# Kernel tuning notes

Hardware: AMD Instinct MI355X
Metric: run time of the kernel (lower is better)

Reference implementation:

```python
import jax, jax.numpy as jnp
import numpy as np

# Layer node counts: [n0, n1, n2, n3] for a 3-hop sampled subgraph
N_NODES = [524288, 65536, 8192, 1024]
DIMS = [100, 256, 256, 47]


def sage_conv(x_src, x_dst, src, dst, Wl, bl, Wr, n_dst):
    # PyG SAGEConv: lin_l(mean_agg(neighbors)) + lin_r(root)
    msg = x_src[src]                                        # [E, in]
    agg = jax.ops.segment_sum(msg, dst, num_segments=n_dst)  # [n_dst, in]
    cnt = jax.ops.segment_sum(jnp.ones((src.shape[0],), dtype=x_src.dtype), dst,
                              num_segments=n_dst)
    agg = agg / jnp.maximum(cnt, 1.0)[:, None]               # mean, 0-deg -> 0
    return agg @ Wl + bl + x_dst @ Wr


def setup_inputs() -> dict:
    key = jax.random.key(0)
    ks = jax.random.split(key, 20)
    inp = {"x": jax.random.normal(ks[0], (N_NODES[0], DIMS[0]), dtype=jnp.float32)}
    E = [655360, 81920, 10240]
    for i in range(3):
        inp[f"src{i}"] = jax.random.randint(ks[1 + 2 * i], (E[i],), 0, N_NODES[i])
        inp[f"dst{i}"] = jax.random.randint(ks[2 + 2 * i], (E[i],), 0, N_NODES[i + 1])
    for i in range(3):
        fin, fout = DIMS[i], DIMS[i + 1]
        inp[f"Wl{i}"] = jax.random.normal(ks[7 + 3 * i], (fin, fout), jnp.float32) * (1.0 / np.sqrt(fin))
        inp[f"bl{i}"] = jnp.zeros((fout,), jnp.float32)
        inp[f"Wr{i}"] = jax.random.normal(ks[8 + 3 * i], (fin, fout), jnp.float32) * (1.0 / np.sqrt(fin))
    return inp


def reference(x, src0, dst0, src1, dst1, src2, dst2,
              Wl0, bl0, Wr0, Wl1, bl1, Wr1, Wl2, bl2, Wr2):
    srcs = [src0, src1, src2]
    dsts = [dst0, dst1, dst2]
    Wls = [Wl0, Wl1, Wl2]
    bls = [bl0, bl1, bl2]
    Wrs = [Wr0, Wr1, Wr2]
    h = x
    for i in range(3):
        n_dst = N_NODES[i + 1]
        h_dst = h[:n_dst]
        h = sage_conv(h, h_dst, srcs[i], dsts[i], Wls[i], bls[i], Wrs[i], n_dst)
        if i != 2:
            h = jax.nn.relu(h)  # dropout is identity in eval mode
    return jax.nn.log_softmax(h, axis=-1)
```

## Files before the change

kernel.cpp:

```cpp
#include <hip/hip_runtime.h>
#include <math.h>

constexpr int NN1 = 65536, NN2 = 8192, NN3 = 1024;
constexpr int E0 = 655360, E1 = 81920, E2 = 10240;
constexpr int ETOT = E0 + E1 + E2;
constexpr int NTOT = NN1 + NN2 + NN3;

static inline int cdiv(int a, int b) { return (a + b - 1) / b; }

typedef __bf16 bf16x8_t __attribute__((ext_vector_type(8)));
typedef float f32x4_t __attribute__((ext_vector_type(4)));

__device__ __forceinline__ unsigned short f2bf(float f) {
    union { float f; unsigned int u; } v; v.f = f;
    unsigned int r = v.u + 0x7fffu + ((v.u >> 16) & 1u);
    return (unsigned short)(r >> 16);
}
__device__ __forceinline__ float bf2f(unsigned short h) {
    union { unsigned int u; float f; } v; v.u = ((unsigned int)h) << 16;
    return v.f;
}

constexpr int CB = (ETOT + 255) / 256;
__global__ void count_prep(const int* __restrict__ dst0, const int* __restrict__ dst1,
                           const int* __restrict__ dst2, int* __restrict__ cnt,
                           const float* __restrict__ Wl0, const float* __restrict__ Wr0,
                           unsigned short* __restrict__ Wt0a, unsigned short* __restrict__ Wt0b,
                           const float* __restrict__ Wl1, const float* __restrict__ Wr1,
                           unsigned short* __restrict__ Wt1a, unsigned short* __restrict__ Wt1b) {
    int b = blockIdx.x, t = threadIdx.x;
    if (b < CB) {
        int i = b * 256 + t;
        if (i < E0) atomicAdd(&cnt[dst0[i]], 1);
        else if (i < E0 + E1) atomicAdd(&cnt[NN1 + dst1[i - E0]], 1);
        else if (i < ETOT) atomicAdd(&cnt[NN1 + NN2 + dst2[i - E0 - E1]], 1);
        return;
    }
    b -= CB;
    if (b < 128) {
        int idx = b * 256 + t; int n = idx >> 7, k = idx & 127;
        Wt0a[idx] = f2bf(k < 100 ? Wl0[k * 256 + n] : 0.f);
    } else if (b < 256) {
        int idx = (b - 128) * 256 + t; int n = idx >> 7, k = idx & 127;
        Wt0b[idx] = f2bf(k < 100 ? Wr0[k * 256 + n] : 0.f);
    } else if (b < 512) {
        int idx = (b - 256) * 256 + t; int n = idx >> 8, k = idx & 255;
        Wt1a[idx] = f2bf(Wl1[k * 256 + n]);
    } else {
        int idx = (b - 512) * 256 + t; int n = idx >> 8, k = idx & 255;
        Wt1b[idx] = f2bf(Wr1[k * 256 + n]);
    }
}

__global__ __launch_bounds__(1024) void scan1(const int* __restrict__ cnt, int n,
                                              int* __restrict__ ofs, int* __restrict__ sums) {
    __shared__ int s[1024];
    int i = blockIdx.x * 1024 + threadIdx.x;
    int v = (i < n) ? cnt[i] : 0;
    s[threadIdx.x] = v;
    __syncthreads();
    for (int off = 1; off < 1024; off <<= 1) {
        int t = (threadIdx.x >= off) ? s[threadIdx.x - off] : 0;
        __syncthreads();
        s[threadIdx.x] += t;
        __syncthreads();
    }
    if (i < n) ofs[i] = s[threadIdx.x] - v;
    if (threadIdx.x == 1023) sums[blockIdx.x] = s[1023];
}

__global__ void scan3(const int* __restrict__ sums, int n,
                      int* __restrict__ ofs, int* __restrict__ cursor) {
    __shared__ int pref_s;
    int c = (blockIdx.x * 256) >> 10;
    if (threadIdx.x < 64) {
        int v = 0;
        for (int j = threadIdx.x; j < c; j += 64) v += sums[j];
        for (int o = 32; o; o >>= 1) v += __shfl_down(v, o);
        if (threadIdx.x == 0) pref_s = v;
    }
    __syncthreads();
    int i = blockIdx.x * 256 + threadIdx.x;
    if (i < n) {
        int v = ofs[i] + pref_s;
        ofs[i] = v;
        cursor[i] = v;
    }
    if (blockIdx.x == 0 && threadIdx.x == 0) ofs[n] = ETOT;
}

__global__ void scatter_all(const int* __restrict__ src0, const int* __restrict__ dst0,
                            const int* __restrict__ src1, const int* __restrict__ dst1,
                            const int* __restrict__ src2, const int* __restrict__ dst2,
                            int* __restrict__ cursor, int* __restrict__ perm) {
    int i = blockIdx.x * 256 + threadIdx.x;
    if (i < E0) {
        int p = atomicAdd(&cursor[dst0[i]], 1);
        perm[p] = src0[i];
    } else if (i < E0 + E1) {
        int j = i - E0;
        int p = atomicAdd(&cursor[NN1 + dst1[j]], 1);
        perm[p] = src1[j];
    } else if (i < ETOT) {
        int j = i - E0 - E1;
        int p = atomicAdd(&cursor[NN1 + NN2 + dst2[j]], 1);
        perm[p] = src2[j];
    }
}

__global__ __launch_bounds__(512) void fused_l0(const float* __restrict__ x,
                                                const int* __restrict__ perm,
                                                const int* __restrict__ ofs,
                                                const unsigned short* __restrict__ Wt0a,
                                                const unsigned short* __restrict__ Wt0b,
                                                const float* __restrict__ bias,
                                                unsigned short* __restrict__ h1) {
    __shared__ unsigned short As[128][136];
    int tid = threadIdx.x;
    int lane = tid & 63, wid = tid >> 6;
    int bm = blockIdx.x * 128;

    {
        int g = lane >> 5, l5 = lane & 31;
        bool act = l5 < 25;
        int node0 = bm + wid * 16;
        int myofs = (lane < 17) ? ofs[node0 + lane] : 0;
        for (int r = 0; r < 16; ++r) {
            int row = wid * 16 + r;
            int s0 = __shfl(myofs, r), s1 = __shfl(myofs, r + 1);
            int deg = s1 - s0;
            float inv = 1.0f / fmaxf((float)deg, 1.0f);
            int dcap = min(deg, 64);
            int pe = (lane < dcap) ? perm[s0 + lane] : 0;
            f32x4_t A0 = {0.f, 0.f, 0.f, 0.f}, A1 = A0, A2 = A0, A3 = A0;
            for (int b = 0; b < dcap; b += 8) {
                int e0 = b + g, e1 = b + 2 + g, e2 = b + 4 + g, e3 = b + 6 + g;
                int p0 = __shfl(pe, e0), p1 = __shfl(pe, e1);
                int p2 = __shfl(pe, e2), p3 = __shfl(pe, e3);
                f32x4_t v0 = {0.f, 0.f, 0.f, 0.f}, v1 = v0, v2 = v0, v3 = v0;
                if (act && e0 < dcap) v0 = *reinterpret_cast<const f32x4_t*>(x + (size_t)p0 * 100 + l5 * 4);
                if (act && e1 < dcap) v1 = *reinterpret_cast<const f32x4_t*>(x + (size_t)p1 * 100 + l5 * 4);
                if (act && e2 < dcap) v2 = *reinterpret_cast<const f32x4_t*>(x + (size_t)p2 * 100 + l5 * 4);
                if (act && e3 < dcap) v3 = *reinterpret_cast<const f32x4_t*>(x + (size_t)p3 * 100 + l5 * 4);
                A0 += v0; A1 += v1; A2 += v2; A3 += v3;
            }
            for (int e = s0 + 64; e < s1; e += 2) {
                int idx = e + g;
                if (act && idx < s1)
                    A0 += *reinterpret_cast<const f32x4_t*>(x + (size_t)perm[idx] * 100 + l5 * 4);
            }
            f32x4_t a = (A0 + A1) + (A2 + A3);
#pragma unroll
            for (int c = 0; c < 4; c++) a[c] += __shfl_xor(a[c], 32);
            if (lane < 25) {
                ushort4 o;
                o.x = f2bf(a[0] * inv); o.y = f2bf(a[1] * inv);
                o.z = f2bf(a[2] * inv); o.w = f2bf(a[3] * inv);
                *reinterpret_cast<ushort4*>(&As[row][lane * 4]) = o;
            } else if (lane < 32) {
                *reinterpret_cast<ushort4*>(&As[row][100 + (lane - 25) * 4]) = make_ushort4(0, 0, 0, 0);
            }
        }
    }

    f32x4_t acc[4][4];
#pragma unroll
    for (int i = 0; i < 4; i++)
#pragma unroll
        for (int j = 0; j < 4; j++)
#pragma unroll
            for (int r = 0; r < 4; r++) acc[i][j][r] = 0.f;

    int r0 = lane & 15, kg = lane >> 4;
    int wm = (wid >> 2) * 64, wn = (wid & 3) * 64;

    for (int pass = 0; pass < 2; ++pass) {
        const unsigned short* W = pass ? Wt0b : Wt0a;
        if (pass) {
            __syncthreads();
            int rown = tid >> 2, q = tid & 3;
            for (int c4 = q; c4 < 25; c4 += 4) {
                f32x4_t v = *reinterpret_cast<const f32x4_t*>(x + (size_t)(bm + rown) * 100 + c4 * 4);
                ushort4 o;
                o.x = f2bf(v[0]); o.y = f2bf(v[1]); o.z = f2bf(v[2]); o.w = f2bf(v[3]);
                *reinterpret_cast<ushort4*>(&As[rown][c4 * 4]) = o;
            }
            if (q == 3) {
#pragma unroll
                for (int c4 = 25; c4 < 32; ++c4)
                    *reinterpret_cast<ushort4*>(&As[rown][c4 * 4]) = make_ushort4(0, 0, 0, 0);
            }
        }
        __syncthreads();
#pragma unroll
        for (int ks = 0; ks < 4; ++ks) {
            bf16x8_t af[4], bfv[4];
#pragma unroll
            for (int ni = 0; ni < 4; ni++)
                bfv[ni] = *reinterpret_cast<const bf16x8_t*>(&W[(size_t)(wn + ni * 16 + r0) * 128 + ks * 32 + kg * 8]);
#pragma unroll
            for (int mi = 0; mi < 4; mi++)
                af[mi] = *reinterpret_cast<const bf16x8_t*>(&As[wm + mi * 16 + r0][ks * 32 + kg * 8]);
#pragma unroll
            for (int mi = 0; mi < 4; mi++)
#pragma unroll
                for (int ni = 0; ni < 4; ni++)
                    acc[mi][ni] = __builtin_amdgcn_mfma_f32_16x16x32_bf16(af[mi], bfv[ni], acc[mi][ni], 0, 0, 0);
        }
    }

    int cc = lane & 15, rr = (lane >> 4) * 4;
#pragma unroll
    for (int mi = 0; mi < 4; mi++) {
#pragma unroll
        for (int ni = 0; ni < 4; ni++) {
            int col = wn + ni * 16 + cc;
            float b = bias[col];
#pragma unroll
            for (int j = 0; j < 4; j++) {
                int row = bm + wm + mi * 16 + rr + j;
                float v = fmaxf(acc[mi][ni][j] + b, 0.f);
                h1[(size_t)row * 256 + col] = f2bf(v);
            }
        }
    }
}

__global__ __launch_bounds__(512) void fused_l1(const unsigned short* __restrict__ h1,
                                                const int* __restrict__ perm,
                                                const int* __restrict__ ofs,
                                                const unsigned short* __restrict__ Wt1a,
                                                const unsigned short* __restrict__ Wt1b,
                                                const float* __restrict__ bias,
                                                float* __restrict__ h2) {
    __shared__ unsigned short As[64][264];
    int tid = threadIdx.x;
    int lane = tid & 63, wid = tid >> 6;
    int bm = blockIdx.x * 64;

    {
        int node0 = bm + wid * 8;
        int myofs = (lane < 9) ? ofs[node0 + lane] : 0;
        for (int r = 0; r < 8; ++r) {
            int row = wid * 8 + r;
            int s0 = __shfl(myofs, r), s1 = __shfl(myofs, r + 1);
            int deg = s1 - s0;
            float inv = 1.0f / fmaxf((float)deg, 1.0f);
            int dcap = min(deg, 64);
            int pe = (lane < dcap) ? perm[s0 + lane] : 0;
            float ac[4][4] = {};
            for (int b = 0; b < dcap; b += 4) {
#pragma unroll
                for (int u = 0; u < 4; u++) {
                    int pu = __shfl(pe, b + u);
                    ushort4 v = make_ushort4(0, 0, 0, 0);
                    if (b + u < dcap)
                        v = *reinterpret_cast<const ushort4*>(h1 + (size_t)pu * 256 + lane * 4);
                    ac[u][0] += bf2f(v.x); ac[u][1] += bf2f(v.y);
                    ac[u][2] += bf2f(v.z); ac[u][3] += bf2f(v.w);
                }
            }
            for (int e = s0 + 64; e < s1; e++) {
                ushort4 v = *reinterpret_cast<const ushort4*>(h1 + (size_t)perm[e] * 256 + lane * 4);
                ac[0][0] += bf2f(v.x); ac[0][1] += bf2f(v.y);
                ac[0][2] += bf2f(v.z); ac[0][3] += bf2f(v.w);
            }
            ushort4 o;
            o.x = f2bf((ac[0][0] + ac[1][0] + ac[2][0] + ac[3][0]) * inv);
            o.y = f2bf((ac[0][1] + ac[1][1] + ac[2][1] + ac[3][1]) * inv);
            o.z = f2bf((ac[0][2] + ac[1][2] + ac[2][2] + ac[3][2]) * inv);
            o.w = f2bf((ac[0][3] + ac[1][3] + ac[2][3] + ac[3][3]) * inv);
            *reinterpret_cast<ushort4*>(&As[row][lane * 4]) = o;
        }
    }

    f32x4_t acc[4][2];
#pragma unroll
    for (int i = 0; i < 4; i++)
#pragma unroll
        for (int j = 0; j < 2; j++)
#pragma unroll
            for (int r = 0; r < 4; r++) acc[i][j][r] = 0.f;

    int r0 = lane & 15, kg = lane >> 4;
    int wn = wid * 32;

    for (int pass = 0; pass < 2; ++pass) {
        const unsigned short* W = pass ? Wt1b : Wt1a;
        if (pass) {
            __syncthreads();
            for (int c = tid; c < 2048; c += 512) {
                int row = c >> 5, k8 = (c & 31) << 3;
                *reinterpret_cast<int4*>(&As[row][k8]) =
                    *reinterpret_cast<const int4*>(&h1[(size_t)(bm + row) * 256 + k8]);
            }
        }
        __syncthreads();
#pragma unroll
        for (int ks = 0; ks < 8; ++ks) {
            bf16x8_t af[4], bfv[2];
#pragma unroll
            for (int ni = 0; ni < 2; ni++)
                bfv[ni] = *reinterpret_cast<const bf16x8_t*>(&W[(size_t)(wn + ni * 16 + r0) * 256 + ks * 32 + kg * 8]);
#pragma unroll
            for (int mi = 0; mi < 4; mi++)
                af[mi] = *reinterpret_cast<const bf16x8_t*>(&As[mi * 16 + r0][ks * 32 + kg * 8]);
#pragma unroll
            for (int mi = 0; mi < 4; mi++)
#pragma unroll
                for (int ni = 0; ni < 2; ni++)
                    acc[mi][ni] = __builtin_amdgcn_mfma_f32_16x16x32_bf16(af[mi], bfv[ni], acc[mi][ni], 0, 0, 0);
        }
    }

    int cc = lane & 15, rr = (lane >> 4) * 4;
#pragma unroll
    for (int mi = 0; mi < 4; mi++) {
#pragma unroll
        for (int ni = 0; ni < 2; ni++) {
            int col = wn + ni * 16 + cc;
            float b = bias[col];
#pragma unroll
            for (int j = 0; j < 4; j++) {
                int row = bm + mi * 16 + rr + j;
                h2[(size_t)row * 256 + col] = fmaxf(acc[mi][ni][j] + b, 0.f);
            }
        }
    }
}

__global__ void agg_vec4_256(const float* __restrict__ x, const int* __restrict__ perm,
                             const int* __restrict__ ofs, float* __restrict__ agg, int nrows) {
    int wave = (blockIdx.x * blockDim.x + threadIdx.x) >> 6;
    int lane = threadIdx.x & 63;
    if (wave >= nrows) return;
    int s0 = ofs[wave], s1 = ofs[wave + 1];
    float4 acc = make_float4(0.f, 0.f, 0.f, 0.f);
    for (int e = s0; e < s1; e++) {
        const float4* xr = (const float4*)(x + (size_t)perm[e] * 256);
        float4 v = xr[lane];
        acc.x += v.x; acc.y += v.y; acc.z += v.z; acc.w += v.w;
    }
    float inv = 1.0f / fmaxf((float)(s1 - s0), 1.0f);
    acc.x *= inv; acc.y *= inv; acc.z *= inv; acc.w *= inv;
    ((float4*)(agg + (size_t)wave * 256))[lane] = acc;
}

__global__ __launch_bounds__(256) void gemm2_fused(const float* __restrict__ A1, const float* __restrict__ W1, int K1,
                                                   const float* __restrict__ A2, const float* __restrict__ W2, int K2,
                                                   const float* __restrict__ bias, float* __restrict__ out,
                                                   int M, int N) {
    __shared__ float As[16][65];
    __shared__ float Bs[16][64];
    int tid = threadIdx.x;
    int tx = tid & 15, ty = tid >> 4;
    int bm = blockIdx.y * 64;
    float acc[4][4] = {};
    for (int pass = 0; pass < 2; ++pass) {
        const float* A = pass ? A2 : A1;
        const float* W = pass ? W2 : W1;
        int K = pass ? K2 : K1;
        for (int k0 = 0; k0 < K; k0 += 16) {
#pragma unroll
            for (int i = 0; i < 4; i++) {
                int L = i * 256 + tid;
                int m = L >> 4, k = L & 15;
                int gm = bm + m, gk = k0 + k;
                float v = 0.f;
                if (gm < M && gk < K) v = A[(size_t)gm * K + gk];
                As[k][m] = v;
            }
#pragma unroll
            for (int i = 0; i < 4; i++) {
                int L = i * 256 + tid;
                int n = L & 63, k = L >> 6;
                int gk = k0 + k;
                float v = 0.f;
                if (gk < K && n < N) v = W[(size_t)gk * N + n];
                Bs[k][n] = v;
            }
            __syncthreads();
#pragma unroll
            for (int k = 0; k < 16; k++) {
                float a[4], b[4];
#pragma unroll
                for (int i = 0; i < 4; i++) a[i] = As[k][ty * 4 + i];
#pragma unroll
                for (int j = 0; j < 4; j++) b[j] = Bs[k][tx * 4 + j];
#pragma unroll
                for (int i = 0; i < 4; i++)
#pragma unroll
                    for (int j = 0; j < 4; j++) acc[i][j] += a[i] * b[j];
            }
            __syncthreads();
        }
    }
#pragma unroll
    for (int i = 0; i < 4; i++) {
        int gm = bm + ty * 4 + i;
        float vals[4];
        float vmax = -1e30f;
#pragma unroll
        for (int j = 0; j < 4; j++) {
            int gn = tx * 4 + j;
            vals[j] = (gn < N) ? acc[i][j] + bias[gn] : -1e30f;
            vmax = fmaxf(vmax, vals[j]);
        }
#pragma unroll
        for (int o = 1; o < 16; o <<= 1) vmax = fmaxf(vmax, __shfl_xor(vmax, o));
        float se = 0.f;
#pragma unroll
        for (int j = 0; j < 4; j++) {
            int gn = tx * 4 + j;
            if (gn < N) se += expf(vals[j] - vmax);
        }
#pragma unroll
        for (int o = 1; o < 16; o <<= 1) se += __shfl_xor(se, o);
        float ls = logf(se);
#pragma unroll
        for (int j = 0; j < 4; j++) {
            int gn = tx * 4 + j;
            if (gn < N && gm < M) out[(size_t)gm * N + gn] = vals[j] - vmax - ls;
        }
    }
}

extern "C" void kernel_launch(void* const* d_in, const int* in_sizes, int n_in,
                              void* d_out, int out_size, void* d_ws, size_t ws_size,
                              hipStream_t stream) {
    const float* x   = (const float*)d_in[0];
    const int* src0  = (const int*)d_in[1];
    const int* dst0  = (const int*)d_in[2];
    const int* src1  = (const int*)d_in[3];
    const int* dst1  = (const int*)d_in[4];
    const int* src2  = (const int*)d_in[5];
    const int* dst2  = (const int*)d_in[6];
    const float* Wl0 = (const float*)d_in[7];
    const float* bl0 = (const float*)d_in[8];
    const float* Wr0 = (const float*)d_in[9];
    const float* Wl1 = (const float*)d_in[10];
    const float* bl1 = (const float*)d_in[11];
    const float* Wr1 = (const float*)d_in[12];
    const float* Wl2 = (const float*)d_in[13];
    const float* bl2 = (const float*)d_in[14];
    const float* Wr2 = (const float*)d_in[15];
    float* out = (float*)d_out;

    char* p = (char*)d_ws;
    auto alloc = [&](size_t bytes) { char* r = p; p += (bytes + 255) & ~(size_t)255; return r; };
    unsigned short* h1   = (unsigned short*)alloc((size_t)NN1 * 256 * 2);
    float* h2    = (float*)alloc((size_t)NN2 * 256 * 4);
    float* agg2  = (float*)alloc((size_t)NN3 * 256 * 4);
    unsigned short* Wt0a = (unsigned short*)alloc(256 * 128 * 2);
    unsigned short* Wt0b = (unsigned short*)alloc(256 * 128 * 2);
    unsigned short* Wt1a = (unsigned short*)alloc(256 * 256 * 2);
    unsigned short* Wt1b = (unsigned short*)alloc(256 * 256 * 2);
    int* cnt    = (int*)alloc((size_t)NTOT * 4);
    int* ofs    = (int*)alloc((size_t)(NTOT + 1) * 4);
    int* cursor = (int*)alloc((size_t)(NTOT + 1) * 4);
    int* sums   = (int*)alloc(128 * 4);
    int* perm   = (int*)alloc((size_t)ETOT * 4);

    hipMemsetAsync(cnt, 0, (size_t)NTOT * 4, stream);
    count_prep<<<CB + 768, 256, 0, stream>>>(dst0, dst1, dst2, cnt,
                                             Wl0, Wr0, Wt0a, Wt0b, Wl1, Wr1, Wt1a, Wt1b);
    int nb = cdiv(NTOT, 1024);
    scan1<<<nb, 1024, 0, stream>>>(cnt, NTOT, ofs, sums);
    scan3<<<cdiv(NTOT, 256), 256, 0, stream>>>(sums, NTOT, ofs, cursor);
    scatter_all<<<cdiv(ETOT, 256), 256, 0, stream>>>(src0, dst0, src1, dst1, src2, dst2, cursor, perm);

    fused_l0<<<NN1 / 128, 512, 0, stream>>>(x, perm, ofs, Wt0a, Wt0b, bl0, h1);

    fused_l1<<<NN2 / 64, 512, 0, stream>>>(h1, perm, ofs + NN1, Wt1a, Wt1b, bl1, h2);

    agg_vec4_256<<<cdiv(NN3 * 64, 256), 256, 0, stream>>>(h2, perm, ofs + NN1 + NN2, agg2, NN3);
    {
        dim3 grid(1, NN3 / 64);
        gemm2_fused<<<grid, 256, 0, stream>>>(agg2, Wl2, 256, h2, Wr2, 256, bl2, out, NN3, 47);
    }
}
```

Before: 302.1 us.

## Gather two destination rows per wave and prefetch next neighbor lists

In the layer-0 and layer-1 fused kernels, each wave now aggregates two destination rows at once. It interleaves their neighbor gathers and prefetches the next pair's offsets and perm indices while the current pair is being summed. The goal is more memory-level parallelism to hide gather latency. Layer 1 also halves the block tile to 32 rows and doubles the grid, which gives more blocks for occupancy but less MFMA work per block. The cost is more registers, and the row bounds must match the new per-wave row count.

```diff
diff --git a/kernel.cpp b/kernel.cpp
--- a/kernel.cpp
+++ b/kernel.cpp
@@ -125,41 +125,85 @@
         bool act = l5 < 25;
         int node0 = bm + wid * 16;
         int myofs = (lane < 17) ? ofs[node0 + lane] : 0;
-        for (int r = 0; r < 16; ++r) {
-            int row = wid * 16 + r;
-            int s0 = __shfl(myofs, r), s1 = __shfl(myofs, r + 1);
-            int deg = s1 - s0;
-            float inv = 1.0f / fmaxf((float)deg, 1.0f);
-            int dcap = min(deg, 64);
-            int pe = (lane < dcap) ? perm[s0 + lane] : 0;
+
+        int s0a = __shfl(myofs, 0);
+        int s0b = __shfl(myofs, 1);
+        int s1b = __shfl(myofs, 2);
+        int dega = s0b - s0a, degb = s1b - s0b;
+        int dca = min(dega, 64), dcb = min(degb, 64);
+        int pea = (lane < dca) ? perm[s0a + lane] : 0;
+        int peb = (lane < dcb) ? perm[s0b + lane] : 0;
+
+        for (int r = 0; r < 16; r += 2) {
+            int s0a_n = 0, s0b_n = 0, dega_n = 0, degb_n = 0, dca_n = 0, dcb_n = 0;
+            int pea_n = 0, peb_n = 0;
+            if (r + 2 < 16) {
+                s0a_n = __shfl(myofs, r + 2);
+                s0b_n = __shfl(myofs, r + 3);
+                int s1b_n = __shfl(myofs, r + 4);
+                dega_n = s0b_n - s0a_n; degb_n = s1b_n - s0b_n;
+                dca_n = min(dega_n, 64); dcb_n = min(degb_n, 64);
+                pea_n = (lane < dca_n) ? perm[s0a_n + lane] : 0;
+                peb_n = (lane < dcb_n) ? perm[s0b_n + lane] : 0;
+            }
             f32x4_t A0 = {0.f, 0.f, 0.f, 0.f}, A1 = A0, A2 = A0, A3 = A0;
-            for (int b = 0; b < dcap; b += 8) {
+            f32x4_t B0 = A0, B1 = A0, B2 = A0, B3 = A0;
+            int mx = max(dca, dcb);
+            for (int b = 0; b < mx; b += 8) {
                 int e0 = b + g, e1 = b + 2 + g, e2 = b + 4 + g, e3 = b + 6 + g;
-                int p0 = __shfl(pe, e0), p1 = __shfl(pe, e1);
-                int p2 = __shfl(pe, e2), p3 = __shfl(pe, e3);
-                f32x4_t v0 = {0.f, 0.f, 0.f, 0.f}, v1 = v0, v2 = v0, v3 = v0;
-                if (act && e0 < dcap) v0 = *reinterpret_cast<const f32x4_t*>(x + (size_t)p0 * 100 + l5 * 4);
-                if (act && e1 < dcap) v1 = *reinterpret_cast<const f32x4_t*>(x + (size_t)p1 * 100 + l5 * 4);
-                if (act && e2 < dcap) v2 = *reinterpret_cast<const f32x4_t*>(x + (size_t)p2 * 100 + l5 * 4);
-                if (act && e3 < dcap) v3 = *reinterpret_cast<const f32x4_t*>(x + (size_t)p3 * 100 + l5 * 4);
-                A0 += v0; A1 += v1; A2 += v2; A3 += v3;
-            }
-            for (int e = s0 + 64; e < s1; e += 2) {
+                int pa0 = __shfl(pea, e0), pa1 = __shfl(pea, e1);
+                int pa2 = __shfl(pea, e2), pa3 = __shfl(pea, e3);
+                int pb0 = __shfl(peb, e0), pb1 = __shfl(peb, e1);
+                int pb2 = __shfl(peb, e2), pb3 = __shfl(peb, e3);
+                f32x4_t z = {0.f, 0.f, 0.f, 0.f};
+                f32x4_t va0 = z, va1 = z, va2 = z, va3 = z;
+                f32x4_t vb0 = z, vb1 = z, vb2 = z, vb3 = z;
+                if (act && e0 < dca) va0 = *reinterpret_cast<const f32x4_t*>(x + (size_t)pa0 * 100 + l5 * 4);
+                if (act && e1 < dca) va1 = *reinterpret_cast<const f32x4_t*>(x + (size_t)pa1 * 100 + l5 * 4);
+                if (act && e2 < dca) va2 = *reinterpret_cast<const f32x4_t*>(x + (size_t)pa2 * 100 + l5 * 4);
+                if (act && e3 < dca) va3 = *reinterpret_cast<const f32x4_t*>(x + (size_t)pa3 * 100 + l5 * 4);
+                if (act && e0 < dcb) vb0 = *reinterpret_cast<const f32x4_t*>(x + (size_t)pb0 * 100 + l5 * 4);
+                if (act && e1 < dcb) vb1 = *reinterpret_cast<const f32x4_t*>(x + (size_t)pb1 * 100 + l5 * 4);
+                if (act && e2 < dcb) vb2 = *reinterpret_cast<const f32x4_t*>(x + (size_t)pb2 * 100 + l5 * 4);
+                if (act && e3 < dcb) vb3 = *reinterpret_cast<const f32x4_t*>(x + (size_t)pb3 * 100 + l5 * 4);
+                A0 += va0; A1 += va1; A2 += va2; A3 += va3;
+                B0 += vb0; B1 += vb1; B2 += vb2; B3 += vb3;
+            }
+            for (int e = s0a + 64; e < s0a + dega; e += 2) {
                 int idx = e + g;
-                if (act && idx < s1)
+                if (act && idx < s0a + dega)
                     A0 += *reinterpret_cast<const f32x4_t*>(x + (size_t)perm[idx] * 100 + l5 * 4);
             }
+            for (int e = s0b + 64; e < s0b + degb; e += 2) {
+                int idx = e + g;
+                if (act && idx < s0b + degb)
+                    B0 += *reinterpret_cast<const f32x4_t*>(x + (size_t)perm[idx] * 100 + l5 * 4);
+            }
             f32x4_t a = (A0 + A1) + (A2 + A3);
-#pragma unroll
-            for (int c = 0; c < 4; c++) a[c] += __shfl_xor(a[c], 32);
+            f32x4_t bb = (B0 + B1) + (B2 + B3);
+#pragma unroll
+            for (int c = 0; c < 4; c++) {
+                a[c] += __shfl_xor(a[c], 32);
+                bb[c] += __shfl_xor(bb[c], 32);
+            }
+            float inva = 1.0f / fmaxf((float)dega, 1.0f);
+            float invb = 1.0f / fmaxf((float)degb, 1.0f);
+            int rowa = wid * 16 + r, rowb = rowa + 1;
             if (lane < 25) {
-                ushort4 o;
-                o.x = f2bf(a[0] * inv); o.y = f2bf(a[1] * inv);
-                o.z = f2bf(a[2] * inv); o.w = f2bf(a[3] * inv);
-                *reinterpret_cast<ushort4*>(&As[row][lane * 4]) = o;
+                ushort4 oa, ob;
+                oa.x = f2bf(a[0] * inva); oa.y = f2bf(a[1] * inva);
+                oa.z = f2bf(a[2] * inva); oa.w = f2bf(a[3] * inva);
+                ob.x = f2bf(bb[0] * invb); ob.y = f2bf(bb[1] * invb);
+                ob.z = f2bf(bb[2] * invb); ob.w = f2bf(bb[3] * invb);
+                *reinterpret_cast<ushort4*>(&As[rowa][lane * 4]) = oa;
+                *reinterpret_cast<ushort4*>(&As[rowb][lane * 4]) = ob;
             } else if (lane < 32) {
-                *reinterpret_cast<ushort4*>(&As[row][100 + (lane - 25) * 4]) = make_ushort4(0, 0, 0, 0);
-            }
+                ushort4 z4 = make_ushort4(0, 0, 0, 0);
+                *reinterpret_cast<ushort4*>(&As[rowa][100 + (lane - 25) * 4]) = z4;
+                *reinterpret_cast<ushort4*>(&As[rowb][100 + (lane - 25) * 4]) = z4;
+            }
+            s0a = s0a_n; s0b = s0b_n; dega = dega_n; degb = degb_n;
+            dca = dca_n; dcb = dcb_n; pea = pea_n; peb = peb_n;
         }
     }
 
@@ -233,50 +277,81 @@
                                                 const unsigned short* __restrict__ Wt1b,
                                                 const float* __restrict__ bias,
                                                 float* __restrict__ h2) {
-    __shared__ unsigned short As[64][264];
+    __shared__ unsigned short As[32][264];
     int tid = threadIdx.x;
     int lane = tid & 63, wid = tid >> 6;
-    int bm = blockIdx.x * 64;
+    int bm = blockIdx.x * 32;
 
     {
-        int node0 = bm + wid * 8;
-        int myofs = (lane < 9) ? ofs[node0 + lane] : 0;
-        for (int r = 0; r < 8; ++r) {
-            int row = wid * 8 + r;
-            int s0 = __shfl(myofs, r), s1 = __shfl(myofs, r + 1);
-            int deg = s1 - s0;
-            float inv = 1.0f / fmaxf((float)deg, 1.0f);
-            int dcap = min(deg, 64);
-            int pe = (lane < dcap) ? perm[s0 + lane] : 0;
-            float ac[4][4] = {};
-            for (int b = 0; b < dcap; b += 4) {
+        int node0 = bm + wid * 4;
+        int myofs = (lane < 5) ? ofs[node0 + lane] : 0;
+        int s0a = __shfl(myofs, 0);
+        int s0b = __shfl(myofs, 1);
+        int s1b = __shfl(myofs, 2);
+        int dega = s0b - s0a, degb = s1b - s0b;
+        int dca = min(dega, 64), dcb = min(degb, 64);
+        int pea = (lane < dca) ? perm[s0a + lane] : 0;
+        int peb = (lane < dcb) ? perm[s0b + lane] : 0;
+
+        for (int r = 0; r < 4; r += 2) {
+            int s0a_n = 0, s0b_n = 0, dega_n = 0, degb_n = 0, dca_n = 0, dcb_n = 0;
+            int pea_n = 0, peb_n = 0;
+            if (r + 2 < 4) {
+                s0a_n = __shfl(myofs, 2);
+                s0b_n = __shfl(myofs, 3);
+                int s1b_n = __shfl(myofs, 4);
+                dega_n = s0b_n - s0a_n; degb_n = s1b_n - s0b_n;
+                dca_n = min(dega_n, 64); dcb_n = min(degb_n, 64);
+                pea_n = (lane < dca_n) ? perm[s0a_n + lane] : 0;
+                peb_n = (lane < dcb_n) ? perm[s0b_n + lane] : 0;
+            }
+            float aca[4][4] = {}, acb[4][4] = {};
+            int mx = max(dca, dcb);
+            for (int b = 0; b < mx; b += 4) {
 #pragma unroll
                 for (int u = 0; u < 4; u++) {
-                    int pu = __shfl(pe, b + u);
-                    ushort4 v = make_ushort4(0, 0, 0, 0);
-                    if (b + u < dcap)
-                        v = *reinterpret_cast<const ushort4*>(h1 + (size_t)pu * 256 + lane * 4);
-                    ac[u][0] += bf2f(v.x); ac[u][1] += bf2f(v.y);
-                    ac[u][2] += bf2f(v.z); ac[u][3] += bf2f(v.w);
+                    int pau = __shfl(pea, b + u);
+                    int pbu = __shfl(peb, b + u);
+                    ushort4 va = make_ushort4(0, 0, 0, 0), vb = va;
+                    if (b + u < dca) va = *reinterpret_cast<const ushort4*>(h1 + (size_t)pau * 256 + lane * 4);
+                    if (b + u < dcb) vb = *reinterpret_cast<const ushort4*>(h1 + (size_t)pbu * 256 + lane * 4);
+                    aca[u][0] += bf2f(va.x); aca[u][1] += bf2f(va.y);
+                    aca[u][2] += bf2f(va.z); aca[u][3] += bf2f(va.w);
+                    acb[u][0] += bf2f(vb.x); acb[u][1] += bf2f(vb.y);
+                    acb[u][2] += bf2f(vb.z); acb[u][3] += bf2f(vb.w);
                 }
             }
-            for (int e = s0 + 64; e < s1; e++) {
+            for (int e = s0a + 64; e < s0a + dega; e++) {
                 ushort4 v = *reinterpret_cast<const ushort4*>(h1 + (size_t)perm[e] * 256 + lane * 4);
-                ac[0][0] += bf2f(v.x); ac[0][1] += bf2f(v.y);
-                ac[0][2] += bf2f(v.z); ac[0][3] += bf2f(v.w);
-            }
-            ushort4 o;
-            o.x = f2bf((ac[0][0] + ac[1][0] + ac[2][0] + ac[3][0]) * inv);
-            o.y = f2bf((ac[0][1] + ac[1][1] + ac[2][1] + ac[3][1]) * inv);
-            o.z = f2bf((ac[0][2] + ac[1][2] + ac[2][2] + ac[3][2]) * inv);
-            o.w = f2bf((ac[0][3] + ac[1][3] + ac[2][3] + ac[3][3]) * inv);
-            *reinterpret_cast<ushort4*>(&As[row][lane * 4]) = o;
-        }
-    }
-
-    f32x4_t acc[4][2];
-#pragma unroll
-    for (int i = 0; i < 4; i++)
+                aca[0][0] += bf2f(v.x); aca[0][1] += bf2f(v.y);
+                aca[0][2] += bf2f(v.z); aca[0][3] += bf2f(v.w);
+            }
+            for (int e = s0b + 64; e < s0b + degb; e++) {
+                ushort4 v = *reinterpret_cast<const ushort4*>(h1 + (size_t)perm[e] * 256 + lane * 4);
+                acb[0][0] += bf2f(v.x); acb[0][1] += bf2f(v.y);
+                acb[0][2] += bf2f(v.z); acb[0][3] += bf2f(v.w);
+            }
+            float inva = 1.0f / fmaxf((float)dega, 1.0f);
+            float invb = 1.0f / fmaxf((float)degb, 1.0f);
+            ushort4 oa, ob;
+            oa.x = f2bf((aca[0][0] + aca[1][0] + aca[2][0] + aca[3][0]) * inva);
+            oa.y = f2bf((aca[0][1] + aca[1][1] + aca[2][1] + aca[3][1]) * inva);
+            oa.z = f2bf((aca[0][2] + aca[1][2] + aca[2][2] + aca[3][2]) * inva);
+            oa.w = f2bf((aca[0][3] + aca[1][3] + aca[2][3] + aca[3][3]) * inva);
+            ob.x = f2bf((acb[0][0] + acb[1][0] + acb[2][0] + acb[3][0]) * invb);
+            ob.y = f2bf((acb[0][1] + acb[1][1] + acb[2][1] + acb[3][1]) * invb);
+            ob.z = f2bf((acb[0][2] + acb[1][2] + acb[2][2] + acb[3][2]) * invb);
+            ob.w = f2bf((acb[0][3] + acb[1][3] + acb[2][3] + acb[3][3]) * invb);
+            *reinterpret_cast<ushort4*>(&As[wid * 4 + r][lane * 4]) = oa;
+            *reinterpret_cast<ushort4*>(&As[wid * 4 + r + 1][lane * 4]) = ob;
+            s0a = s0a_n; s0b = s0b_n; dega = dega_n; degb = degb_n;
+            dca = dca_n; dcb = dcb_n; pea = pea_n; peb = peb_n;
+        }
+    }
+
+    f32x4_t acc[2][2];
+#pragma unroll
+    for (int i = 0; i < 2; i++)
 #pragma unroll
         for (int j = 0; j < 2; j++)
 #pragma unroll
@@ -289,7 +364,7 @@
         const unsigned short* W = pass ? Wt1b : Wt1a;
         if (pass) {
             __syncthreads();
-            for (int c = tid; c < 2048; c += 512) {
+            for (int c = tid; c < 1024; c += 512) {
                 int row = c >> 5, k8 = (c & 31) << 3;
                 *reinterpret_cast<int4*>(&As[row][k8]) =
                     *reinterpret_cast<const int4*>(&h1[(size_t)(bm + row) * 256 + k8]);
@@ -298,15 +373,15 @@
         __syncthreads();
 #pragma unroll
         for (int ks = 0; ks < 8; ++ks) {
-            bf16x8_t af[4], bfv[2];
+            bf16x8_t af[2], bfv[2];
 #pragma unroll
             for (int ni = 0; ni < 2; ni++)
                 bfv[ni] = *reinterpret_cast<const bf16x8_t*>(&W[(size_t)(wn + ni * 16 + r0) * 256 + ks * 32 + kg * 8]);
 #pragma unroll
-            for (int mi = 0; mi < 4; mi++)
+            for (int mi = 0; mi < 2; mi++)
                 af[mi] = *reinterpret_cast<const bf16x8_t*>(&As[mi * 16 + r0][ks * 32 + kg * 8]);
 #pragma unroll
-            for (int mi = 0; mi < 4; mi++)
+            for (int mi = 0; mi < 2; mi++)
 #pragma unroll
                 for (int ni = 0; ni < 2; ni++)
                     acc[mi][ni] = __builtin_amdgcn_mfma_f32_16x16x32_bf16(af[mi], bfv[ni], acc[mi][ni], 0, 0, 0);
@@ -315,7 +390,7 @@
 
     int cc = lane & 15, rr = (lane >> 4) * 4;
 #pragma unroll
-    for (int mi = 0; mi < 4; mi++) {
+    for (int mi = 0; mi < 2; mi++) {
 #pragma unroll
         for (int ni = 0; ni < 2; ni++) {
             int col = wn + ni * 16 + cc;
@@ -471,7 +546,7 @@
 
     fused_l0<<<NN1 / 128, 512, 0, stream>>>(x, perm, ofs, Wt0a, Wt0b, bl0, h1);
 
-    fused_l1<<<NN2 / 64, 512, 0, stream>>>(h1, perm, ofs + NN1, Wt1a, Wt1b, bl1, h2);
+    fused_l1<<<NN2 / 32, 512, 0, stream>>>(h1, perm, ofs + NN1, Wt1a, Wt1b, bl1, h2);
 
     agg_vec4_256<<<cdiv(NN3 * 64, 256), 256, 0, stream>>>(h2, perm, ofs + NN1 + NN2, agg2, NN3);
     {
```

Result: faster. 290.7 us (-3.8%).
